# Performance work log

Hardware: AMD Instinct MI355X
Metric: run time of the kernel (lower is better)

The kernel has to match this reference:

```python
import jax, jax.numpy as jnp
import numpy as np

EMBED_DIM = 1024
NUM_HEADS = 16
HEAD_DIM = EMBED_DIM // NUM_HEADS
ROPE_BASE = 10000.0


def rotate_half(x):
    d = x.shape[-1] // 2
    x1, x2 = x[..., :d], x[..., d:]
    return jnp.concatenate((-x2, x1), axis=-1)


def setup_inputs() -> dict:
    key = jax.random.key(0)
    k_x, k_wqkv, k_bqkv, k_wo, k_bo = jax.random.split(key, 5)
    C = EMBED_DIM
    x = jax.random.normal(k_x, (4, 2048, C), dtype=jnp.float32)
    s = 1.0 / np.sqrt(C)
    W_qkv = jax.random.uniform(k_wqkv, (C, 3 * C), minval=-s, maxval=s, dtype=jnp.float32)
    b_qkv = jax.random.uniform(k_bqkv, (3 * C,), minval=-s, maxval=s, dtype=jnp.float32)
    W_out = jax.random.uniform(k_wo, (C, C), minval=-s, maxval=s, dtype=jnp.float32)
    b_out = jax.random.uniform(k_bo, (C,), minval=-s, maxval=s, dtype=jnp.float32)
    return {"x": x, "W_qkv": W_qkv, "b_qkv": b_qkv, "W_out": W_out, "b_out": b_out}


def reference(x, W_qkv, b_qkv, W_out, b_out):
    B, T, C = x.shape
    H, Dh = NUM_HEADS, HEAD_DIM
    # fused QKV projection: [B,T,3C] -> [3,B,H,T,Dh]
    qkv = (x @ W_qkv + b_qkv).reshape(B, T, 3, H, Dh).transpose(2, 0, 3, 1, 4)
    q, k, v = qkv[0], qkv[1], qkv[2]
    # rotary embedding: freqs [T, Dh/2] -> emb [T, Dh]
    inv_freq = 1.0 / (ROPE_BASE ** (jnp.arange(0, Dh, 2, dtype=jnp.float32) / Dh))
    freqs = jnp.arange(T, dtype=jnp.float32)[:, None] * inv_freq[None, :]
    emb = jnp.concatenate((freqs, freqs), axis=-1)  # [T, Dh], broadcasts over B,H
    cos, sin = jnp.cos(emb), jnp.sin(emb)
    q = q * cos + rotate_half(q) * sin
    k = k * cos + rotate_half(k) * sin
    # full (non-causal) attention, manual softmax
    scale = 1.0 / np.sqrt(Dh)
    attn = jax.nn.softmax(jnp.einsum("bhqd,bhkd->bhqk", q, k) * scale, axis=-1)
    out = jnp.einsum("bhqk,bhkd->bhqd", attn, v)  # [B,H,T,Dh]
    out = out.transpose(0, 2, 1, 3).reshape(B, T, C)
    return out @ W_out + b_out
```

## Files before the change

kernel.cpp:

```cpp
#include <hip/hip_runtime.h>
#include <math.h>

#define T_SEQ 2048
#define CDIM  1024
#define NH    16
#define DHD   64
#define BATCH 4
#define MROWS (BATCH * T_SEQ)
#define BHN   (BATCH * NH)

typedef _Float16 f16;
typedef __attribute__((ext_vector_type(8))) _Float16 f16x8;
typedef __attribute__((ext_vector_type(4))) _Float16 f16x4;
typedef __attribute__((ext_vector_type(2))) _Float16 f16x2;
typedef __attribute__((ext_vector_type(2))) __fp16 fp16x2;
typedef __attribute__((ext_vector_type(4))) float f32x4;
typedef __attribute__((ext_vector_type(16))) float f32x16;
typedef __attribute__((ext_vector_type(4))) unsigned int uint4v;

__device__ __forceinline__ float fast_exp2(float x) {
#if __has_builtin(__builtin_amdgcn_exp2f)
    return __builtin_amdgcn_exp2f(x);
#else
    return exp2f(x);
#endif
}

__device__ __forceinline__ float fast_rcp(float x) {
#if __has_builtin(__builtin_amdgcn_rcpf)
    return __builtin_amdgcn_rcpf(x);
#else
    return 1.0f / x;
#endif
}

__device__ __forceinline__ f16x2 cvt_pk_f16(float a, float b) {
    fp16x2 r = __builtin_amdgcn_cvt_pkrtz(a, b);
    return __builtin_bit_cast(f16x2, r);
}

__device__ __forceinline__ void permlane32_swap(unsigned &a, unsigned &b) {
    asm volatile("v_permlane32_swap_b32 %0, %1" : "+v"(a), "+v"(b));
}

__device__ __forceinline__ void gl_lds16(const f16* g, f16* l) {
    __builtin_amdgcn_global_load_lds(
        (const __attribute__((address_space(1))) void*)(g),
        (__attribute__((address_space(3))) void*)(l),
        16, 0, 0);
}

__global__ __launch_bounds__(256) void prep_kernel(
    const float* __restrict__ X, f16* __restrict__ Xf,
    const float* __restrict__ Wq, const float* __restrict__ Wo,
    f16* __restrict__ Wqt, f16* __restrict__ Wot,
    float* __restrict__ ctab, float* __restrict__ stab)
{
    const int bx = blockIdx.x;
    if (bx < 256) {
        int idx = bx * 256 + threadIdx.x;
        int t = idx >> 5, i = idx & 31;
        double inv = pow(10000.0, -(double)(2 * i) / 64.0);
        double a = (double)t * inv;
        ctab[idx] = (float)cos(a);
        stab[idx] = (float)sin(a);
    } else if (bx < 4352) {
        int idx = (bx - 256) * 256 + threadIdx.x;
        const float4* src = (const float4*)X + (size_t)idx * 2;
        float4 a = src[0], b = src[1];
        f16x8 o;
        o[0] = (f16)a.x; o[1] = (f16)a.y; o[2] = (f16)a.z; o[3] = (f16)a.w;
        o[4] = (f16)b.x; o[5] = (f16)b.y; o[6] = (f16)b.z; o[7] = (f16)b.w;
        *((f16x8*)Xf + idx) = o;
    } else {
        const int sub = threadIdx.x >> 6, lane = threadIdx.x & 63;
        const int id = (bx - 4352) * 4 + sub;
        const int k0 = (id & 127) * 8;
        const int ny = id >> 7;
        const float* W;
        f16* Wt;
        int N, n;
        if (ny < 48) { W = Wq; Wt = Wqt; N = 3072; n = ny * 64 + lane; }
        else         { W = Wo; Wt = Wot; N = 1024; n = (ny - 48) * 64 + lane; }
        f16x8 o;
#pragma unroll
        for (int j = 0; j < 8; j++) o[j] = (f16)W[(size_t)(k0 + j) * N + n];
        *(f16x8*)(Wt + (size_t)n * CDIM + k0) = o;
    }
}

#define GEMM_MAINLOOP(Aimg, Bimg, M0, N0)                                         \
    __shared__ f16 As[128][64], Bs[128][64];                                      \
    const int tid = threadIdx.x, wave = tid >> 6, lane = tid & 63;                \
    const int l16 = lane & 15, quad = lane >> 4;                                  \
    const int wm = wave >> 1, wn = wave & 1;                                      \
    f32x4 acc[4][4];                                                              \
    _Pragma("unroll") for (int i = 0; i < 4; i++)                                 \
        _Pragma("unroll") for (int j = 0; j < 4; j++)                             \
            acc[i][j] = (f32x4){0.f, 0.f, 0.f, 0.f};                              \
    const f16* sbase = (wave < 2) ? (Aimg) : (Bimg);                              \
    f16* lbase = ((wave < 2) ? &As[0][0] : &Bs[0][0]) + (wave & 1) * 4096;        \
    const size_t srow0 = ((wave < 2) ? (size_t)(M0) : (size_t)(N0)) + (wave & 1) * 64; \
    const int srow = lane >> 3, schunk = lane & 7;                                \
    const int gchunk = (schunk ^ srow) << 3;         \
    for (int k0 = 0; k0 < CDIM; k0 += 64) {                                       \
        _Pragma("unroll") for (int it = 0; it < 8; it++)                          \
            gl_lds16(sbase + (srow0 + it * 8 + srow) * CDIM + k0 + gchunk,        \
                     lbase + it * 512);                                           \
        __syncthreads();                                                          \
        _Pragma("unroll") for (int ks = 0; ks < 2; ks++) {                        \
            f16x8 fa[4], fb[4];                                                   \
            _Pragma("unroll") for (int mi = 0; mi < 4; mi++)                      \
                fa[mi] = *(const f16x8*)                                          \
                    &As[wm * 64 + mi * 16 + l16][((ks * 4 + quad) ^ (l16 & 7)) << 3]; \
            _Pragma("unroll") for (int ni = 0; ni < 4; ni++)                      \
                fb[ni] = *(const f16x8*)                                          \
                    &Bs[wn * 64 + ni * 16 + l16][((ks * 4 + quad) ^ (l16 & 7)) << 3]; \
            _Pragma("unroll") for (int mi = 0; mi < 4; mi++)                      \
                _Pragma("unroll") for (int ni = 0; ni < 4; ni++)                  \
                    acc[mi][ni] = __builtin_amdgcn_mfma_f32_16x16x32_f16(         \
                        fa[mi], fb[ni], acc[mi][ni], 0, 0, 0);                    \
        }                                                                         \
        __syncthreads();                                                          \
    }

__global__ __launch_bounds__(256) void qkv_gemm_kernel(
    const f16* __restrict__ Xf, const f16* __restrict__ Wt,
    const float* __restrict__ bias,
    const float* __restrict__ ctab, const float* __restrict__ stab,
    f16* __restrict__ qf, f16* __restrict__ kf, f16* __restrict__ vtb)
{
    const int m0 = blockIdx.x * 128;
    const int n0 = blockIdx.y * 128;
    GEMM_MAINLOOP(Xf, Wt, m0, n0)

    const int ncol0 = n0 + wn * 64;
    const int w = ncol0 >> 10;
    const int h = (ncol0 >> 6) & 15;
    const int b = m0 >> 11;
    const int trow0 = (m0 & 2047) + wm * 64 + quad * 4;
    float bia[4];
#pragma unroll
    for (int ni = 0; ni < 4; ni++) bia[ni] = bias[ncol0 + ni * 16 + l16];

    if (w < 2) {
        f16* oq = w ? kf : qf;
        const float sc = w ? 1.0f : 0.18033688011112042f;
#pragma unroll
        for (int mi = 0; mi < 4; mi++) {
#pragma unroll
            for (int i = 0; i < 4; i++) {
                int t = trow0 + mi * 16 + i;
                size_t rowoff = ((size_t)(b * NH + h) * T_SEQ + t) * DHD;
#pragma unroll
                for (int np = 0; np < 2; np++) {
                    int d = np * 16 + l16;
                    float v0 = acc[mi][np][i] + bia[np];
                    float v1 = acc[mi][np + 2][i] + bia[np + 2];
                    float c = ctab[(t << 5) + d];
                    float s = stab[(t << 5) + d];
                    oq[rowoff + d]      = (f16)((v0 * c - v1 * s) * sc);
                    oq[rowoff + d + 32] = (f16)((v1 * c + v0 * s) * sc);
                }
            }
        }
    } else {
#pragma unroll
        for (int mi = 0; mi < 4; mi++) {
            const int tb = trow0 + mi * 16;
#pragma unroll
            for (int ni = 0; ni < 4; ni++) {
                const int d = ni * 16 + l16;
                f16x4 pv;
#pragma unroll
                for (int i = 0; i < 4; i++) pv[i] = (f16)(acc[mi][ni][i] + bia[ni]);
                *(f16x4*)(vtb + ((size_t)(b * NH + h) * DHD + d) * T_SEQ + tb) = pv;
            }
        }
    }
}

__global__ __launch_bounds__(256, 4) void attn_kernel(
    const f16* __restrict__ qf, const f16* __restrict__ kf,
    const f16* __restrict__ vt, f16* __restrict__ ab)
{
    __shared__ f16 Kb[2][64][64];
    __shared__ f16 Vb[2][64][64];
    __shared__ float Lb[4][32];

    const int tid  = threadIdx.x;
    const int wave = tid >> 6, lane = tid & 63;
    const int l31  = lane & 31, hh = lane >> 5;

    const int flat = blockIdx.x + (blockIdx.y << 4);
    const int swz  = (flat & 7) * 128 + (flat >> 3);
    const int qt = swz & 15;
    const int bh = swz >> 4;
    const int q0 = qt * 128 + wave * 32;

    const f16* kbase = kf + (size_t)bh * T_SEQ * DHD;
    const f16* vbase = vt + (size_t)bh * DHD * T_SEQ;

    f16x8 qfr[4];
    {
        const f16* qrow = qf + ((size_t)bh * T_SEQ + q0 + l31) * DHD + hh * 8;
#pragma unroll
        for (int kk = 0; kk < 4; kk++)
            qfr[kk] = *(const f16x8*)(qrow + kk * 16);
    }

    f32x16 o[2];
#pragma unroll
    for (int db = 0; db < 2; db++)
#pragma unroll
        for (int r = 0; r < 16; r++) o[db][r] = 0.f;
    float lacc = 0.f;

    const int srow = tid >> 3;
    const int schunk = tid & 7;
    const int gcol = (schunk ^ (srow & 7)) << 3;

#define STAGE(t, b)                                                               \
    {                                                                             \
        const f16* kg = kbase + ((size_t)(t) * 64 + srow) * DHD + gcol;           \
        const f16* vg = vbase + (size_t)srow * T_SEQ + (t) * 64 + gcol;           \
        f16* kl = &Kb[b][wave * 8][0];                                            \
        f16* vl = &Vb[b][wave * 8][0];                                            \
        gl_lds16(kg, kl);                                                         \
        gl_lds16(kg + 32 * DHD, kl + 32 * 64);                                    \
        gl_lds16(vg, vl);                                                         \
        gl_lds16(vg + (size_t)32 * T_SEQ, vl + 32 * 64);                          \
    }

    STAGE(0, 0)
    __syncthreads();

    for (int kt = 0; kt < 32; kt++) {
        const int buf = kt & 1;
        if (kt < 31) STAGE(kt + 1, buf ^ 1)

        f16x8 pA[4];
#pragma unroll
        for (int b2 = 0; b2 < 2; b2++) {
            f32x16 scc;
#pragma unroll
            for (int r = 0; r < 16; r++) scc[r] = 0.f;
            __builtin_amdgcn_s_setprio(1);
#pragma unroll
            for (int kk = 0; kk < 4; kk++) {
                const int kc = ((kk * 2 + hh) ^ (l31 & 7)) << 3;
                f16x8 kfr = *(const f16x8*)&Kb[buf][b2 * 32 + l31][kc];
                scc = __builtin_amdgcn_mfma_f32_32x32x16_f16(
                    kfr, qfr[kk], scc, 0, 0, 0);
            }
            __builtin_amdgcn_s_setprio(0);
            float e[16];
#pragma unroll
            for (int r = 0; r < 16; r++) {
                e[r] = fast_exp2(scc[r]);
                lacc += e[r];
            }
            unsigned pk[8];
#pragma unroll
            for (int i = 0; i < 8; i++)
                pk[i] = __builtin_bit_cast(unsigned,
                                           cvt_pk_f16(e[2 * i], e[2 * i + 1]));
            permlane32_swap(pk[0], pk[2]);
            permlane32_swap(pk[1], pk[3]);
            permlane32_swap(pk[4], pk[6]);
            permlane32_swap(pk[5], pk[7]);
            uint4v a0 = {pk[0], pk[1], pk[2], pk[3]};
            uint4v a1 = {pk[4], pk[5], pk[6], pk[7]};
            pA[b2 * 2]     = __builtin_bit_cast(f16x8, a0);
            pA[b2 * 2 + 1] = __builtin_bit_cast(f16x8, a1);
        }
        __builtin_amdgcn_s_setprio(1);
#pragma unroll
        for (int db = 0; db < 2; db++) {
#pragma unroll
            for (int kk = 0; kk < 4; kk++) {
                const int vc = ((kk * 2 + hh) ^ (l31 & 7)) << 3;
                f16x8 vfr = *(const f16x8*)&Vb[buf][db * 32 + l31][vc];
                o[db] = __builtin_amdgcn_mfma_f32_32x32x16_f16(
                    pA[kk], vfr, o[db], 0, 0, 0);
            }
        }
        __builtin_amdgcn_s_setprio(0);

        if (kt < 31) __syncthreads();
    }
#undef STAGE

    lacc += __shfl_xor(lacc, 32);
    if (lane < 32) Lb[wave][l31] = lacc;
    __syncthreads();
    f32x4 ivv[4];
#pragma unroll
    for (int g = 0; g < 4; g++)
        ivv[g] = *(const f32x4*)&Lb[wave][g * 8 + hh * 4];

    const int b = bh >> 4, h = bh & 15;
#pragma unroll
    for (int r = 0; r < 16; r++) {
        const int qrow = (r & 3) + 8 * (r >> 2) + 4 * hh;
        const int m = b * T_SEQ + qt * 128 + wave * 32 + qrow;
        const float iv = fast_rcp(ivv[r >> 2][r & 3]);
        f16* dst = ab + (size_t)m * CDIM + h * 64 + l31;
        dst[0]  = (f16)(o[0][r] * iv);
        dst[32] = (f16)(o[1][r] * iv);
    }
}

__global__ __launch_bounds__(256) void out_gemm_kernel(
    const f16* __restrict__ Ab, const f16* __restrict__ Wt,
    const float* __restrict__ bias, float* __restrict__ out)
{
    const int m0 = blockIdx.x * 128;
    const int n0 = blockIdx.y * 128;
    GEMM_MAINLOOP(Ab, Wt, m0, n0)

    const int ncol0 = n0 + wn * 64;
    float bia[4];
#pragma unroll
    for (int ni = 0; ni < 4; ni++) bia[ni] = bias[ncol0 + ni * 16 + l16];
#pragma unroll
    for (int mi = 0; mi < 4; mi++) {
#pragma unroll
        for (int i = 0; i < 4; i++) {
            int m = m0 + wm * 64 + mi * 16 + quad * 4 + i;
#pragma unroll
            for (int ni = 0; ni < 4; ni++)
                out[(size_t)m * CDIM + ncol0 + ni * 16 + l16] = acc[mi][ni][i] + bia[ni];
        }
    }
}

extern "C" void kernel_launch(void* const* d_in, const int* in_sizes, int n_in,
                              void* d_out, int out_size, void* d_ws, size_t ws_size,
                              hipStream_t stream)
{
    const float* x    = (const float*)d_in[0];
    const float* Wqkv = (const float*)d_in[1];
    const float* bqkv = (const float*)d_in[2];
    const float* Wout = (const float*)d_in[3];
    const float* bout = (const float*)d_in[4];
    float* out = (float*)d_out;

    const size_t XSZ  = (size_t)MROWS * CDIM;
    const size_t WQSZ = (size_t)3072 * CDIM;
    const size_t WOSZ = (size_t)CDIM * CDIM;
    const size_t QSZ  = (size_t)BHN * T_SEQ * DHD;

    char* p = (char*)d_ws;
    f16* Xf  = (f16*)p; p += XSZ * 2;
    f16* Wqt = (f16*)p; p += WQSZ * 2;
    f16* Wot = (f16*)p; p += WOSZ * 2;
    f16* qf  = (f16*)p; p += QSZ * 2;
    f16* kf  = (f16*)p; p += QSZ * 2;
    f16* vtb = (f16*)p; p += QSZ * 2;
    f16* ab  = (f16*)p; p += QSZ * 2;
    float* ctab = (float*)p; p += T_SEQ * 32 * 4;
    float* stab = (float*)p; p += T_SEQ * 32 * 4;

    prep_kernel<<<6400, 256, 0, stream>>>(x, Xf, Wqkv, Wout, Wqt, Wot, ctab, stab);
    qkv_gemm_kernel<<<dim3(64, 24), 256, 0, stream>>>(
        Xf, Wqt, bqkv, ctab, stab, qf, kf, vtb);
    attn_kernel<<<dim3(16, BHN), 256, 0, stream>>>(qf, kf, vtb, ab);
    out_gemm_kernel<<<dim3(64, 8), 256, 0, stream>>>(ab, Wot, bout, out);
}
```

Baseline: 276.7 us.

## Double per-wave query rows in attention and stage K/V through registers

Each wave now handles 64 query rows (two 32-row groups) instead of 32, so each K/V fragment read from LDS feeds two MFMAs and the grid halves to 8 query tiles per head. The async global-to-LDS copy is replaced by register-staged loads: the next tile is fetched into registers at the top of the iteration and written to LDS after compute. This trades higher register use (launch bounds lowered to 2 blocks) and fewer blocks for reduced K/V traffic per query.

```diff
diff --git a/kernel.cpp b/kernel.cpp
--- a/kernel.cpp
+++ b/kernel.cpp
@@ -180,99 +180,121 @@
     }
 }
 
-__global__ __launch_bounds__(256, 4) void attn_kernel(
+__global__ __launch_bounds__(256, 2) void attn_kernel(
     const f16* __restrict__ qf, const f16* __restrict__ kf,
     const f16* __restrict__ vt, f16* __restrict__ ab)
 {
     __shared__ f16 Kb[2][64][64];
     __shared__ f16 Vb[2][64][64];
-    __shared__ float Lb[4][32];
+    __shared__ float Lb[4][2][32];
 
     const int tid  = threadIdx.x;
     const int wave = tid >> 6, lane = tid & 63;
     const int l31  = lane & 31, hh = lane >> 5;
 
-    const int flat = blockIdx.x + (blockIdx.y << 4);
-    const int swz  = (flat & 7) * 128 + (flat >> 3);
-    const int qt = swz & 15;
-    const int bh = swz >> 4;
-    const int q0 = qt * 128 + wave * 32;
+    const int flat = blockIdx.x + (blockIdx.y << 3);
+    const int swz  = (flat & 7) * 64 + (flat >> 3);
+    const int qt = swz & 7;
+    const int bh = swz >> 3;
+    const int q0 = qt * 256 + wave * 64;
 
     const f16* kbase = kf + (size_t)bh * T_SEQ * DHD;
     const f16* vbase = vt + (size_t)bh * DHD * T_SEQ;
 
-    f16x8 qfr[4];
-    {
-        const f16* qrow = qf + ((size_t)bh * T_SEQ + q0 + l31) * DHD + hh * 8;
+    f16x8 qfr[2][4];
+#pragma unroll
+    for (int g = 0; g < 2; g++) {
+        const f16* qrow = qf + ((size_t)bh * T_SEQ + q0 + g * 32 + l31) * DHD + hh * 8;
 #pragma unroll
         for (int kk = 0; kk < 4; kk++)
-            qfr[kk] = *(const f16x8*)(qrow + kk * 16);
-    }
-
-    f32x16 o[2];
-#pragma unroll
-    for (int db = 0; db < 2; db++)
-#pragma unroll
-        for (int r = 0; r < 16; r++) o[db][r] = 0.f;
-    float lacc = 0.f;
+            qfr[g][kk] = *(const f16x8*)(qrow + kk * 16);
+    }
+
+    f32x16 o[2][2];
+#pragma unroll
+    for (int g = 0; g < 2; g++)
+#pragma unroll
+        for (int db = 0; db < 2; db++)
+#pragma unroll
+            for (int r = 0; r < 16; r++) o[g][db][r] = 0.f;
+    float lacc[2] = {0.f, 0.f};
 
     const int srow = tid >> 3;
-    const int schunk = tid & 7;
-    const int gcol = (schunk ^ (srow & 7)) << 3;
-
-#define STAGE(t, b)                                                               \
-    {                                                                             \
-        const f16* kg = kbase + ((size_t)(t) * 64 + srow) * DHD + gcol;           \
-        const f16* vg = vbase + (size_t)srow * T_SEQ + (t) * 64 + gcol;           \
-        f16* kl = &Kb[b][wave * 8][0];                                            \
-        f16* vl = &Vb[b][wave * 8][0];                                            \
-        gl_lds16(kg, kl);                                                         \
-        gl_lds16(kg + 32 * DHD, kl + 32 * 64);                                    \
-        gl_lds16(vg, vl);                                                         \
-        gl_lds16(vg + (size_t)32 * T_SEQ, vl + 32 * 64);                          \
-    }
-
-    STAGE(0, 0)
+    const int scw  = tid & 7;
+    const int scol = scw << 3;
+    const int swzc = (scw ^ (srow & 7)) << 3;
+
+    const f16* kp = kbase + (size_t)srow * DHD + scol;
+    const f16* vp = vbase + (size_t)srow * T_SEQ + scol;
+
+    f16x8 kreg[2], vreg[2];
+#pragma unroll
+    for (int r = 0; r < 2; r++) {
+        kreg[r] = *(const f16x8*)(kp + (size_t)(r * 32) * DHD);
+        vreg[r] = *(const f16x8*)(vp + (size_t)(r * 32) * T_SEQ);
+    }
+#pragma unroll
+    for (int r = 0; r < 2; r++) {
+        *(f16x8*)&Kb[0][srow + r * 32][swzc] = kreg[r];
+        *(f16x8*)&Vb[0][srow + r * 32][swzc] = vreg[r];
+    }
+    const f16* kq = kp + 64 * DHD;
+    const f16* vq = vp + 64;
     __syncthreads();
 
     for (int kt = 0; kt < 32; kt++) {
         const int buf = kt & 1;
-        if (kt < 31) STAGE(kt + 1, buf ^ 1)
-
-        f16x8 pA[4];
+        if (kt < 31) {
+#pragma unroll
+            for (int r = 0; r < 2; r++) {
+                kreg[r] = *(const f16x8*)(kq + (size_t)(r * 32) * DHD);
+                vreg[r] = *(const f16x8*)(vq + (size_t)(r * 32) * T_SEQ);
+            }
+            kq += 64 * DHD;
+            vq += 64;
+        }
+
+        f16x8 pA[2][4];
 #pragma unroll
         for (int b2 = 0; b2 < 2; b2++) {
-            f32x16 scc;
-#pragma unroll
-            for (int r = 0; r < 16; r++) scc[r] = 0.f;
+            f32x16 scc[2];
+#pragma unroll
+            for (int g = 0; g < 2; g++)
+#pragma unroll
+                for (int r = 0; r < 16; r++) scc[g][r] = 0.f;
             __builtin_amdgcn_s_setprio(1);
 #pragma unroll
             for (int kk = 0; kk < 4; kk++) {
                 const int kc = ((kk * 2 + hh) ^ (l31 & 7)) << 3;
                 f16x8 kfr = *(const f16x8*)&Kb[buf][b2 * 32 + l31][kc];
-                scc = __builtin_amdgcn_mfma_f32_32x32x16_f16(
-                    kfr, qfr[kk], scc, 0, 0, 0);
+                scc[0] = __builtin_amdgcn_mfma_f32_32x32x16_f16(
+                    kfr, qfr[0][kk], scc[0], 0, 0, 0);
+                scc[1] = __builtin_amdgcn_mfma_f32_32x32x16_f16(
+                    kfr, qfr[1][kk], scc[1], 0, 0, 0);
             }
             __builtin_amdgcn_s_setprio(0);
-            float e[16];
-#pragma unroll
-            for (int r = 0; r < 16; r++) {
-                e[r] = fast_exp2(scc[r]);
-                lacc += e[r];
-            }
-            unsigned pk[8];
-#pragma unroll
-            for (int i = 0; i < 8; i++)
-                pk[i] = __builtin_bit_cast(unsigned,
-                                           cvt_pk_f16(e[2 * i], e[2 * i + 1]));
-            permlane32_swap(pk[0], pk[2]);
-            permlane32_swap(pk[1], pk[3]);
-            permlane32_swap(pk[4], pk[6]);
-            permlane32_swap(pk[5], pk[7]);
-            uint4v a0 = {pk[0], pk[1], pk[2], pk[3]};
-            uint4v a1 = {pk[4], pk[5], pk[6], pk[7]};
-            pA[b2 * 2]     = __builtin_bit_cast(f16x8, a0);
-            pA[b2 * 2 + 1] = __builtin_bit_cast(f16x8, a1);
+#pragma unroll
+            for (int g = 0; g < 2; g++) {
+                float e[16];
+#pragma unroll
+                for (int r = 0; r < 16; r++) {
+                    e[r] = fast_exp2(scc[g][r]);
+                    lacc[g] += e[r];
+                }
+                unsigned pk[8];
+#pragma unroll
+                for (int i = 0; i < 8; i++)
+                    pk[i] = __builtin_bit_cast(unsigned,
+                                               cvt_pk_f16(e[2 * i], e[2 * i + 1]));
+                permlane32_swap(pk[0], pk[2]);
+                permlane32_swap(pk[1], pk[3]);
+                permlane32_swap(pk[4], pk[6]);
+                permlane32_swap(pk[5], pk[7]);
+                uint4v a0 = {pk[0], pk[1], pk[2], pk[3]};
+                uint4v a1 = {pk[4], pk[5], pk[6], pk[7]};
+                pA[g][b2 * 2]     = __builtin_bit_cast(f16x8, a0);
+                pA[g][b2 * 2 + 1] = __builtin_bit_cast(f16x8, a1);
+            }
         }
         __builtin_amdgcn_s_setprio(1);
 #pragma unroll
@@ -281,33 +303,47 @@
             for (int kk = 0; kk < 4; kk++) {
                 const int vc = ((kk * 2 + hh) ^ (l31 & 7)) << 3;
                 f16x8 vfr = *(const f16x8*)&Vb[buf][db * 32 + l31][vc];
-                o[db] = __builtin_amdgcn_mfma_f32_32x32x16_f16(
-                    pA[kk], vfr, o[db], 0, 0, 0);
+                o[0][db] = __builtin_amdgcn_mfma_f32_32x32x16_f16(
+                    pA[0][kk], vfr, o[0][db], 0, 0, 0);
+                o[1][db] = __builtin_amdgcn_mfma_f32_32x32x16_f16(
+                    pA[1][kk], vfr, o[1][db], 0, 0, 0);
             }
         }
         __builtin_amdgcn_s_setprio(0);
 
-        if (kt < 31) __syncthreads();
-    }
-#undef STAGE
-
-    lacc += __shfl_xor(lacc, 32);
-    if (lane < 32) Lb[wave][l31] = lacc;
+        if (kt < 31) {
+#pragma unroll
+            for (int r = 0; r < 2; r++) {
+                *(f16x8*)&Kb[buf ^ 1][srow + r * 32][swzc] = kreg[r];
+                *(f16x8*)&Vb[buf ^ 1][srow + r * 32][swzc] = vreg[r];
+            }
+            __syncthreads();
+        }
+    }
+
+#pragma unroll
+    for (int g = 0; g < 2; g++) {
+        lacc[g] += __shfl_xor(lacc[g], 32);
+        if (lane < 32) Lb[wave][g][l31] = lacc[g];
+    }
     __syncthreads();
-    f32x4 ivv[4];
-#pragma unroll
-    for (int g = 0; g < 4; g++)
-        ivv[g] = *(const f32x4*)&Lb[wave][g * 8 + hh * 4];
 
     const int b = bh >> 4, h = bh & 15;
 #pragma unroll
-    for (int r = 0; r < 16; r++) {
-        const int qrow = (r & 3) + 8 * (r >> 2) + 4 * hh;
-        const int m = b * T_SEQ + qt * 128 + wave * 32 + qrow;
-        const float iv = fast_rcp(ivv[r >> 2][r & 3]);
-        f16* dst = ab + (size_t)m * CDIM + h * 64 + l31;
-        dst[0]  = (f16)(o[0][r] * iv);
-        dst[32] = (f16)(o[1][r] * iv);
+    for (int g = 0; g < 2; g++) {
+        f32x4 ivv[4];
+#pragma unroll
+        for (int j = 0; j < 4; j++)
+            ivv[j] = *(const f32x4*)&Lb[wave][g][j * 8 + hh * 4];
+#pragma unroll
+        for (int r = 0; r < 16; r++) {
+            const int qrow = (r & 3) + 8 * (r >> 2) + 4 * hh;
+            const int m = b * T_SEQ + qt * 256 + wave * 64 + g * 32 + qrow;
+            const float iv = fast_rcp(ivv[r >> 2][r & 3]);
+            f16* dst = ab + (size_t)m * CDIM + h * 64 + l31;
+            dst[0]  = (f16)(o[g][0][r] * iv);
+            dst[32] = (f16)(o[g][1][r] * iv);
+        }
     }
 }
 
@@ -365,6 +401,6 @@
     prep_kernel<<<6400, 256, 0, stream>>>(x, Xf, Wqkv, Wout, Wqt, Wot, ctab, stab);
     qkv_gemm_kernel<<<dim3(64, 24), 256, 0, stream>>>(
         Xf, Wqt, bqkv, ctab, stab, qf, kf, vtb);
-    attn_kernel<<<dim3(16, BHN), 256, 0, stream>>>(qf, kf, vtb, ab);
+    attn_kernel<<<dim3(8, BHN), 256, 0, stream>>>(qf, kf, vtb, ab);
     out_gemm_kernel<<<dim3(64, 8), 256, 0, stream>>>(ab, Wot, bout, out);
 }
```

Result: no change. 280.4 us (+1.3%).

## Rewrite QKV GEMM with 256x256 tiles, 512 threads and double-buffered LDS prefetch

Applied to the files above, without the earlier changes.

Replaces the shared 128x128 GEMM mainloop in the QKV projection with a dedicated 256x256-tile kernel of 8 waves. It double-buffers LDS with direct global-to-LDS loads issued two k-steps ahead, and interleaves MFMA with barriers using s_setprio. This raises data reuse per tile and overlaps loads with compute. The cost is 128 KB of LDS per block, more accumulator registers, and only 384 blocks, which may hurt occupancy and tail balance.

```diff
diff --git a/kernel.cpp b/kernel.cpp
--- a/kernel.cpp
+++ b/kernel.cpp
@@ -124,21 +124,93 @@
         __syncthreads();                                                          \
     }
 
-__global__ __launch_bounds__(256) void qkv_gemm_kernel(
+__global__ __launch_bounds__(512, 2) void qkv_gemm_kernel(
     const f16* __restrict__ Xf, const f16* __restrict__ Wt,
     const float* __restrict__ bias,
     const float* __restrict__ ctab, const float* __restrict__ stab,
     f16* __restrict__ qf, f16* __restrict__ kf, f16* __restrict__ vtb)
 {
-    const int m0 = blockIdx.x * 128;
-    const int n0 = blockIdx.y * 128;
-    GEMM_MAINLOOP(Xf, Wt, m0, n0)
-
-    const int ncol0 = n0 + wn * 64;
+    __shared__ f16 As[2][256][64], Bs[2][256][64];
+
+    const int tid = threadIdx.x, wave = tid >> 6, lane = tid & 63;
+    const int l16 = lane & 15, quad = lane >> 4;
+    const int wr = wave >> 2, wc = wave & 3;
+    const int m0 = blockIdx.x * 256;
+    const int n0 = blockIdx.y * 256;
+
+    f32x4 acc[8][4];
+#pragma unroll
+    for (int i = 0; i < 8; i++)
+#pragma unroll
+        for (int j = 0; j < 4; j++) acc[i][j] = (f32x4){0.f, 0.f, 0.f, 0.f};
+
+    const int srow = tid >> 3;
+    const int gch  = ((tid & 7) ^ (srow & 7)) << 3;
+    const int lrow0 = srow & 56;
+
+#define STG(kt, b)                                                                 \
+    {                                                                              \
+        const int k0_ = (kt) * 64;                                                 \
+        _Pragma("unroll") for (int it = 0; it < 4; it++) {                         \
+            gl_lds16(Xf + (size_t)(m0 + it * 64 + srow) * CDIM + k0_ + gch,        \
+                     &As[b][it * 64 + lrow0][0]);                                  \
+            gl_lds16(Wt + (size_t)(n0 + it * 64 + srow) * CDIM + k0_ + gch,        \
+                     &Bs[b][it * 64 + lrow0][0]);                                  \
+        }                                                                          \
+    }
+
+    STG(0, 0)
+    STG(1, 1)
+    asm volatile("s_waitcnt vmcnt(8)" ::: "memory");
+    __builtin_amdgcn_s_barrier();
+
+    for (int t = 0; t < 16; t++) {
+        const int buf = t & 1;
+        f16x8 fb[4][2];
+#pragma unroll
+        for (int p = 0; p < 4; p++) {
+            if (p == 0) {
+#pragma unroll
+                for (int ni = 0; ni < 4; ni++)
+#pragma unroll
+                    for (int kk = 0; kk < 2; kk++)
+                        fb[ni][kk] = *(const f16x8*)
+                            &Bs[buf][wc * 64 + ni * 16 + l16][((kk * 4 + quad) ^ (l16 & 7)) << 3];
+            }
+            f16x8 fa[2][2];
+#pragma unroll
+            for (int m2 = 0; m2 < 2; m2++)
+#pragma unroll
+                for (int kk = 0; kk < 2; kk++)
+                    fa[m2][kk] = *(const f16x8*)
+                        &As[buf][wr * 128 + (p * 2 + m2) * 16 + l16][((kk * 4 + quad) ^ (l16 & 7)) << 3];
+            __builtin_amdgcn_s_setprio(1);
+#pragma unroll
+            for (int kk = 0; kk < 2; kk++)
+#pragma unroll
+                for (int m2 = 0; m2 < 2; m2++)
+#pragma unroll
+                    for (int ni = 0; ni < 4; ni++)
+                        acc[p * 2 + m2][ni] = __builtin_amdgcn_mfma_f32_16x16x32_f16(
+                            fa[m2][kk], fb[ni][kk], acc[p * 2 + m2][ni], 0, 0, 0);
+            __builtin_amdgcn_s_setprio(0);
+            __builtin_amdgcn_s_barrier();
+        }
+        if (t < 14) {
+            STG(t + 2, buf)
+            asm volatile("s_waitcnt vmcnt(8)" ::: "memory");
+        } else if (t == 14) {
+            asm volatile("s_waitcnt vmcnt(0)" ::: "memory");
+        }
+        if (t < 15) __builtin_amdgcn_s_barrier();
+    }
+#undef STG
+
+    const int ncol0 = n0 + wc * 64;
     const int w = ncol0 >> 10;
     const int h = (ncol0 >> 6) & 15;
     const int b = m0 >> 11;
-    const int trow0 = (m0 & 2047) + wm * 64 + quad * 4;
+    const int trow0 = (m0 & 2047) + wr * 128 + quad * 4;
     float bia[4];
 #pragma unroll
     for (int ni = 0; ni < 4; ni++) bia[ni] = bias[ncol0 + ni * 16 + l16];
@@ -147,7 +219,7 @@
         f16* oq = w ? kf : qf;
         const float sc = w ? 1.0f : 0.18033688011112042f;
 #pragma unroll
-        for (int mi = 0; mi < 4; mi++) {
+        for (int mi = 0; mi < 8; mi++) {
 #pragma unroll
             for (int i = 0; i < 4; i++) {
                 int t = trow0 + mi * 16 + i;
@@ -166,7 +238,7 @@
         }
     } else {
 #pragma unroll
-        for (int mi = 0; mi < 4; mi++) {
+        for (int mi = 0; mi < 8; mi++) {
             const int tb = trow0 + mi * 16;
 #pragma unroll
             for (int ni = 0; ni < 4; ni++) {
@@ -363,7 +435,7 @@
     float* stab = (float*)p; p += T_SEQ * 32 * 4;
 
     prep_kernel<<<6400, 256, 0, stream>>>(x, Xf, Wqkv, Wout, Wqt, Wot, ctab, stab);
-    qkv_gemm_kernel<<<dim3(64, 24), 256, 0, stream>>>(
+    qkv_gemm_kernel<<<dim3(32, 12), 512, 0, stream>>>(
         Xf, Wqt, bqkv, ctab, stab, qf, kf, vtb);
     attn_kernel<<<dim3(16, BHN), 256, 0, stream>>>(qf, kf, vtb, ab);
     out_gemm_kernel<<<dim3(64, 8), 256, 0, stream>>>(ab, Wot, bout, out);
```

Result: no change. 276.9 us (+0.1%).
